# Kernel optimization log

Hardware: AMD Instinct MI355X
Metric: run time of the kernel (lower is better)

## Reference

```python
import jax, jax.numpy as jnp
import numpy as np

N_USER = 50000
N_ITEM = 50000
N = N_USER + N_ITEM
EMB = 64
FEAT = 64
LAYERS = [128, 128]   # input_dim = EMB + FEAT = 128
NNZ = 3_200_000
BATCH = 4096
NEG_SLOPE = 0.2
EPS = 1e-12


def setup_inputs() -> dict:
    key = jax.random.key(0)
    ks = jax.random.split(key, 16)
    inp = {}
    # forward index args
    inp["users"] = jax.random.randint(ks[0], (BATCH,), 0, N_USER)
    inp["pos_items"] = jax.random.randint(ks[1], (BATCH,), 0, N_ITEM)
    inp["neg_items"] = jax.random.randint(ks[2], (BATCH,), 0, N_ITEM)
    # learned embeddings (xavier-ish scale)
    inp["user_emb"] = jax.random.normal(ks[3], (N_USER, EMB), jnp.float32) * 0.1
    inp["item_emb1"] = jax.random.normal(ks[4], (N_ITEM, EMB), jnp.float32) * 0.1
    inp["item_emb2"] = jax.random.normal(ks[5], (N_ITEM, FEAT), jnp.float32) * 0.1
    # fixed user feature matrix (densified sparse feature, non-trainable)
    inp["feature"] = jax.random.normal(ks[6], (N_USER, FEAT), jnp.float32) * 0.1
    # hop-mixing scalar weights w1,w2,w3 (softmax(alpha) at init, then free params)
    alpha = jax.random.normal(ks[7], (3,), jnp.float32)
    inp["w"] = jax.nn.softmax(alpha)
    # per-layer GC / BI weights (all 128x128 here, so stack)
    din = EMB + FEAT
    sc = 1.0 / np.sqrt(din)
    K = len(LAYERS)
    inp["W_gc"] = jax.random.uniform(ks[8], (K, din, LAYERS[0]), jnp.float32, -sc, sc)
    inp["b_gc"] = jax.random.uniform(ks[9], (K, 1, LAYERS[0]), jnp.float32, -sc, sc)
    inp["W_bi"] = jax.random.uniform(ks[10], (K, din, LAYERS[0]), jnp.float32, -sc, sc)
    inp["b_bi"] = jax.random.uniform(ks[11], (K, 1, LAYERS[0]), jnp.float32, -sc, sc)
    # normalized adjacency in COO form (same sparsity pattern for all hops)
    inp["adj_rows"] = jax.random.randint(ks[12], (NNZ,), 0, N)
    inp["adj_cols"] = jax.random.randint(ks[13], (NNZ,), 0, N)
    inp["adj_vals"] = jax.random.uniform(ks[14], (NNZ,), jnp.float32, 0.0, 0.06)
    return inp


def _spmm(vals, rows, cols, X):
    # sparse (N,N) @ dense (N,D) via gather + segment-sum
    return jax.ops.segment_sum(vals[:, None] * X[cols], rows, num_segments=N)


def _forward(users, pos_items, neg_items, user_emb, item_emb1, item_emb2,
             feature, w, W_gc, b_gc, W_bi, b_bi, adj_rows, adj_cols, adj_vals):
    temp = jnp.concatenate([feature, item_emb2], axis=0)            # (N, FEAT)
    ego = jnp.concatenate([user_emb, item_emb1], axis=0)            # (N, EMB)
    ego = jnp.concatenate([ego, temp], axis=1)                      # (N, 128)
    all_emb = [ego]
    # torch `A ** i` cumulative -> elementwise value powers v, v^2, v^6
    v = adj_vals
    comb = w[0] * v + w[1] * (v ** 2) + w[2] * (v ** 6)
    for k in range(len(LAYERS)):
        side = _spmm(comb, adj_rows, adj_cols, ego)                 # (N, 128)
        sum_e = side @ W_gc[k] + b_gc[k]
        bi_e = (ego * side) @ W_bi[k] + b_bi[k]
        ego = jax.nn.leaky_relu(sum_e + bi_e, negative_slope=NEG_SLOPE)
        nrm = jnp.linalg.norm(ego, axis=1, keepdims=True)
        all_emb.append(ego / jnp.maximum(nrm, EPS))                 # F.normalize
    all_e = jnp.concatenate(all_emb, axis=1)                        # (N, 384)
    u_g = all_e[:N_USER][users]
    pos_g = all_e[N_USER:][pos_items]
    neg_g = all_e[N_USER:][neg_items]
    return u_g, pos_g, neg_g


def reference(users, pos_items, neg_items, user_emb, item_emb1, item_emb2,
              feature, w, W_gc, b_gc, W_bi, b_bi, adj_rows, adj_cols, adj_vals):
    return _forward(users, pos_items, neg_items, user_emb, item_emb1, item_emb2,
                    feature, w, W_gc, b_gc, W_bi, b_bi, adj_rows, adj_cols, adj_vals)
```

## Files before the change

### kernel.cpp

```cpp
#include <hip/hip_runtime.h>
#include <math.h>

#define N_USER 50000
#define N_ITEM 50000
#define NTOT   100000
#define D      128
#define BATCH_ 4096
#define NEG_SLOPE 0.2f
#define EPS_ 1e-12f
#define SCAN_CHUNK 1024
#define NBUK 782
#define NCHK 256
#define NSCAN (NBUK * NCHK)
#define BUKCAP 12288

typedef __attribute__((ext_vector_type(8))) short bfrag;
typedef __attribute__((ext_vector_type(4))) float f32x4;

static __device__ __forceinline__ float bf2f(unsigned short h) {
    return __uint_as_float(((unsigned)h) << 16);
}
static __device__ __forceinline__ unsigned short f2bf(float f) {
    unsigned u = __float_as_uint(f);
    u += 0x7fffu + ((u >> 16) & 1u);
    return (unsigned short)(u >> 16);
}

__global__ void assemble_and_pack(const float* __restrict__ user_emb,
                                  const float* __restrict__ item_emb1,
                                  const float* __restrict__ item_emb2,
                                  const float* __restrict__ feature,
                                  const float* __restrict__ W_gc,
                                  const float* __restrict__ W_bi,
                                  unsigned short* __restrict__ ego0h,
                                  unsigned short* __restrict__ Wp) {
    if (blockIdx.x < 32) {
        int t = blockIdx.x * 256 + threadIdx.x;
        int lane  = t & 63;
        int nt    = (t >> 6) & 7;
        int kt    = (t >> 9) & 3;
        int mat   = (t >> 11) & 1;
        int layer = (t >> 12) & 1;
        const float* W = (mat ? W_bi : W_gc) + (size_t)layer * D * D;
        int n = nt * 16 + (lane & 15);
        int kbase = kt * 32 + (lane >> 4) * 8;
        unsigned short o8[8];
        #pragma unroll
        for (int e = 0; e < 8; ++e) o8[e] = f2bf(W[(size_t)(kbase + e) * D + n]);
        *(int4*)(Wp + (size_t)t * 8) = *(int4*)o8;
        return;
    }
    int t = (blockIdx.x - 32) * 256 + threadIdx.x;
    const int total = NTOT * (D / 4);
    if (t >= total) return;
    int row = t >> 5;
    int q   = t & 31;
    int d0  = q * 4;
    const float* src;
    if (d0 < 64) {
        src = (row < N_USER) ? user_emb  + (size_t)row * 64 + d0
                             : item_emb1 + (size_t)(row - N_USER) * 64 + d0;
    } else {
        src = (row < N_USER) ? feature   + (size_t)row * 64 + (d0 - 64)
                             : item_emb2 + (size_t)(row - N_USER) * 64 + (d0 - 64);
    }
    float4 v = *(const float4*)src;
    ushort4 h;
    h.x = f2bf(v.x); h.y = f2bf(v.y); h.z = f2bf(v.z); h.w = f2bf(v.w);
    *(ushort4*)(ego0h + (size_t)row * D + d0) = h;
}

__global__ __launch_bounds__(1024) void hist_buckets(const int* __restrict__ rows,
                                                     int* __restrict__ cnt2,
                                                     int nnz, int chunk_sz) {
    __shared__ int h[NBUK];
    for (int i = threadIdx.x; i < NBUK; i += 1024) h[i] = 0;
    __syncthreads();
    int c = blockIdx.x;
    int base = c * chunk_sz, end = min(base + chunk_sz, nnz);
    for (int e = base + threadIdx.x; e < end; e += 1024)
        atomicAdd(&h[rows[e] >> 7], 1);
    __syncthreads();
    for (int b = threadIdx.x; b < NBUK; b += 1024)
        cnt2[b * NCHK + c] = h[b];
}

__global__ __launch_bounds__(1024) void scan_block_sums(const int* __restrict__ cnt,
                                                        int* __restrict__ bsum, int n) {
    __shared__ int ws[16];
    int i = blockIdx.x * SCAN_CHUNK + threadIdx.x;
    int x = (i < n) ? cnt[i] : 0;
    #pragma unroll
    for (int d = 32; d >= 1; d >>= 1) x += __shfl_xor(x, d);
    int wid = threadIdx.x >> 6, lane = threadIdx.x & 63;
    if (lane == 0) ws[wid] = x;
    __syncthreads();
    if (threadIdx.x == 0) {
        int s = 0;
        #pragma unroll
        for (int k = 0; k < 16; ++k) s += ws[k];
        bsum[blockIdx.x] = s;
    }
}

__global__ void scan_small(const int* __restrict__ bsum, int* __restrict__ boff, int nb) {
    if (threadIdx.x == 0 && blockIdx.x == 0) {
        int acc = 0;
        for (int i = 0; i < nb; ++i) { boff[i] = acc; acc += bsum[i]; }
    }
}

__global__ __launch_bounds__(1024) void scan_chunks(const int* __restrict__ cnt,
                                                    const int* __restrict__ boff,
                                                    int* __restrict__ off, int n) {
    __shared__ int ws[16];
    int tid = threadIdx.x;
    int i = blockIdx.x * SCAN_CHUNK + tid;
    int x = (i < n) ? cnt[i] : 0;
    int v = x;
    #pragma unroll
    for (int d = 1; d < 64; d <<= 1) { int u = __shfl_up(v, d); if ((tid & 63) >= d) v += u; }
    int wid = tid >> 6, lane = tid & 63;
    if (lane == 63) ws[wid] = v;
    __syncthreads();
    if (wid == 0) {
        int s = (lane < 16) ? ws[lane] : 0;
        #pragma unroll
        for (int d = 1; d < 16; d <<= 1) { int u = __shfl_up(s, d); if (lane >= d) s += u; }
        if (lane < 16) ws[lane] = s;
    }
    __syncthreads();
    int woff = (wid == 0) ? 0 : ws[wid - 1];
    if (i < n) off[i] = boff[blockIdx.x] + woff + v - x;
}

__global__ __launch_bounds__(1024) void partition_edges(
        const int* __restrict__ rows, const int* __restrict__ cols,
        const float* __restrict__ vals, const float* __restrict__ w3,
        const int* __restrict__ scanout, int2* __restrict__ tmp8,
        int nnz, int chunk_sz) {
    __shared__ int cur[NBUK];
    int c = blockIdx.x;
    for (int b = threadIdx.x; b < NBUK; b += 1024) cur[b] = scanout[b * NCHK + c];
    __syncthreads();
    const float w0 = w3[0], w1 = w3[1], w2 = w3[2];
    int base = c * chunk_sz, end = min(base + chunk_sz, nnz);
    for (int e = base + threadIdx.x; e < end; e += 1024) {
        int r = rows[e];
        float v = vals[e];
        float v2 = v * v;
        float comb = w0 * v + w1 * v2 + w2 * v2 * v2 * v2;
        int pos = atomicAdd(&cur[r >> 7], 1);
        tmp8[pos] = make_int2(((r & 127) << 17) | cols[e], __float_as_int(comb));
    }
}

__global__ __launch_bounds__(256) void bucket_sort(
        const int2* __restrict__ tmp8, const int* __restrict__ scanout,
        unsigned* __restrict__ edges4, int* __restrict__ row_off, int nnz) {
    __shared__ int hist[128], exc[129], cur[128];
    __shared__ unsigned st[BUKCAP];
    int b = blockIdx.x;
    int lo = scanout[b * NCHK];
    int hi = (b + 1 < NBUK) ? scanout[(b + 1) * NCHK] : nnz;
    int cnt = hi - lo;
    if (threadIdx.x < 128) hist[threadIdx.x] = 0;
    __syncthreads();
    for (int i = lo + threadIdx.x; i < hi; i += 256)
        atomicAdd(&hist[tmp8[i].x >> 17], 1);
    __syncthreads();
    if (threadIdx.x == 0) {
        int a = 0;
        for (int r = 0; r < 128; ++r) { exc[r] = a; a += hist[r]; }
        exc[128] = a;
    }
    __syncthreads();
    if (threadIdx.x < 128) {
        cur[threadIdx.x] = exc[threadIdx.x];
        int grow = b * 128 + threadIdx.x;
        if (grow <= NTOT) row_off[grow] = lo + exc[threadIdx.x];
    }
    __syncthreads();
    if (cnt <= BUKCAP) {
        for (int i = lo + threadIdx.x; i < hi; i += 256) {
            int2 t = tmp8[i];
            int rl = t.x >> 17;
            int p = atomicAdd(&cur[rl], 1);
            unsigned cb = (unsigned)f2bf(__int_as_float(t.y)) & 0x7FFFu;
            st[p] = (cb << 17) | ((unsigned)t.x & 0x1FFFFu);
        }
        __syncthreads();
        for (int i = threadIdx.x; i < cnt; i += 256)
            edges4[lo + i] = st[i];
    } else {
        for (int i = lo + threadIdx.x; i < hi; i += 256) {
            int2 t = tmp8[i];
            int rl = t.x >> 17;
            int p = atomicAdd(&cur[rl], 1);
            unsigned cb = (unsigned)f2bf(__int_as_float(t.y)) & 0x7FFFu;
            edges4[lo + p] = (cb << 17) | ((unsigned)t.x & 0x1FFFFu);
        }
    }
}

__global__ __launch_bounds__(256) void spmm_csr_h(const int* __restrict__ row_off,
                                                  const unsigned* __restrict__ edges4,
                                                  const unsigned short* __restrict__ Xh,
                                                  unsigned short* __restrict__ side_h) {
    int row = (blockIdx.x * blockDim.x + threadIdx.x) >> 6;
    if (row >= NTOT) return;
    int lane = threadIdx.x & 63;
    int g = lane >> 4;
    int q = lane & 15;
    int s = row_off[row], e = row_off[row + 1];

    float a[8];
    #pragma unroll
    for (int j = 0; j < 8; ++j) a[j] = 0.f;

    for (int i = s; i < e; i += 16) {
        int i0 = i + g, i1 = i + 4 + g, i2 = i + 8 + g, i3 = i + 12 + g;
        unsigned e0 = (i0 < e) ? edges4[i0] : 0u;
        unsigned e1 = (i1 < e) ? edges4[i1] : 0u;
        unsigned e2 = (i2 < e) ? edges4[i2] : 0u;
        unsigned e3 = (i3 < e) ? edges4[i3] : 0u;
        float v0 = bf2f((unsigned short)(e0 >> 17));
        float v1 = bf2f((unsigned short)(e1 >> 17));
        float v2 = bf2f((unsigned short)(e2 >> 17));
        float v3 = bf2f((unsigned short)(e3 >> 17));
        int4 x0 = *(const int4*)(Xh + (size_t)(e0 & 0x1FFFFu) * D + q * 8);
        int4 x1 = *(const int4*)(Xh + (size_t)(e1 & 0x1FFFFu) * D + q * 8);
        int4 x2 = *(const int4*)(Xh + (size_t)(e2 & 0x1FFFFu) * D + q * 8);
        int4 x3 = *(const int4*)(Xh + (size_t)(e3 & 0x1FFFFu) * D + q * 8);
        const unsigned short* p0 = (const unsigned short*)&x0;
        const unsigned short* p1 = (const unsigned short*)&x1;
        const unsigned short* p2 = (const unsigned short*)&x2;
        const unsigned short* p3 = (const unsigned short*)&x3;
        #pragma unroll
        for (int j = 0; j < 8; ++j)
            a[j] += v0 * bf2f(p0[j]) + v1 * bf2f(p1[j])
                  + v2 * bf2f(p2[j]) + v3 * bf2f(p3[j]);
    }
    #pragma unroll
    for (int j = 0; j < 8; ++j) {
        a[j] += __shfl_xor(a[j], 16);
        a[j] += __shfl_xor(a[j], 32);
    }
    if (g == 0) {
        unsigned short o[8];
        #pragma unroll
        for (int j = 0; j < 8; ++j) o[j] = f2bf(a[j]);
        *(int4*)(side_h + (size_t)row * D + q * 8) = *(int4*)o;
    }
}

__global__ __launch_bounds__(256) void layer_gemm_mfma(
        const unsigned short* __restrict__ side_h,
        const unsigned short* __restrict__ ego_h,
        const unsigned short* __restrict__ Wp, int layer,
        const float* __restrict__ bgc, const float* __restrict__ bbi,
        unsigned short* __restrict__ ego_out_h, float* __restrict__ norms) {
    __shared__ unsigned short Sl[64 * D];
    __shared__ unsigned short Pl[64 * D];
    __shared__ float sqp[4][64];

    const int r0  = blockIdx.x * 64;
    const int tid = threadIdx.x;
    const int lane = tid & 63;
    const int wv   = tid >> 6;

    #pragma unroll
    for (int it = 0; it < 4; ++it) {
        int c = tid + it * 256;
        int r = c >> 4;
        int q = c & 15;
        int row = r0 + r;
        int4 sv = make_int4(0, 0, 0, 0), ev = make_int4(0, 0, 0, 0);
        if (row < NTOT) {
            sv = *(const int4*)(side_h + (size_t)row * D + q * 8);
            ev = *(const int4*)(ego_h  + (size_t)row * D + q * 8);
        }
        int dst = (r * 256 + q * 16) ^ ((r & 7) << 4);
        *(int4*)((char*)Sl + dst) = sv;
        const unsigned short* sp = (const unsigned short*)&sv;
        const unsigned short* ep = (const unsigned short*)&ev;
        unsigned short pv[8];
        #pragma unroll
        for (int j = 0; j < 8; ++j) pv[j] = f2bf(bf2f(sp[j]) * bf2f(ep[j]));
        *(int4*)((char*)Pl + dst) = *(int4*)pv;
    }

    bfrag wg[4][2], wb[4][2];
    #pragma unroll
    for (int kt = 0; kt < 4; ++kt)
        #pragma unroll
        for (int n2 = 0; n2 < 2; ++n2) {
            int nt = wv * 2 + n2;
            size_t og = ((((size_t)(layer * 2 + 0) * 4 + kt) * 8 + nt) * 64 + lane) * 8;
            size_t ob = ((((size_t)(layer * 2 + 1) * 4 + kt) * 8 + nt) * 64 + lane) * 8;
            wg[kt][n2] = *(const bfrag*)(Wp + og);
            wb[kt][n2] = *(const bfrag*)(Wp + ob);
        }

    __syncthreads();

    f32x4 acc[4][2];
    #pragma unroll
    for (int m = 0; m < 4; ++m)
        #pragma unroll
        for (int n = 0; n < 2; ++n) acc[m][n] = (f32x4){0.f, 0.f, 0.f, 0.f};

    #pragma unroll
    for (int kt = 0; kt < 4; ++kt) {
        bfrag sf[4], pf[4];
        #pragma unroll
        for (int m = 0; m < 4; ++m) {
            int rowl = m * 16 + (lane & 15);
            int byte = (rowl * 256 + kt * 64 + (lane >> 4) * 16) ^ ((rowl & 7) << 4);
            sf[m] = *(const bfrag*)((const char*)Sl + byte);
            pf[m] = *(const bfrag*)((const char*)Pl + byte);
        }
        #pragma unroll
        for (int m = 0; m < 4; ++m)
            #pragma unroll
            for (int n = 0; n < 2; ++n) {
                acc[m][n] = __builtin_amdgcn_mfma_f32_16x16x32_bf16(sf[m], wg[kt][n], acc[m][n], 0, 0, 0);
                acc[m][n] = __builtin_amdgcn_mfma_f32_16x16x32_bf16(pf[m], wb[kt][n], acc[m][n], 0, 0, 0);
            }
    }

    float bsum[2];
    #pragma unroll
    for (int n = 0; n < 2; ++n) {
        int col = wv * 32 + n * 16 + (lane & 15);
        bsum[n] = bgc[col] + bbi[col];
    }

    float sq[4][4];
    #pragma unroll
    for (int m = 0; m < 4; ++m)
        #pragma unroll
        for (int r = 0; r < 4; ++r) sq[m][r] = 0.f;

    #pragma unroll
    for (int m = 0; m < 4; ++m) {
        int rowl = m * 16 + (lane >> 4) * 4;
        #pragma unroll
        for (int n = 0; n < 2; ++n) {
            int col = wv * 32 + n * 16 + (lane & 15);
            #pragma unroll
            for (int r = 0; r < 4; ++r) {
                float o = acc[m][n][r] + bsum[n];
                o = (o > 0.f) ? o : NEG_SLOPE * o;
                sq[m][r] += o * o;
                int row = r0 + rowl + r;
                if (row < NTOT)
                    ego_out_h[(size_t)row * D + col] = f2bf(o);
            }
        }
    }

    #pragma unroll
    for (int m = 0; m < 4; ++m)
        #pragma unroll
        for (int r = 0; r < 4; ++r) {
            float v = sq[m][r];
            #pragma unroll
            for (int off = 8; off >= 1; off >>= 1) v += __shfl_xor(v, off);
            if ((lane & 15) == 0) sqp[wv][m * 16 + (lane >> 4) * 4 + r] = v;
        }
    __syncthreads();
    if (tid < 64) {
        int row = r0 + tid;
        if (row < NTOT) {
            float s = sqp[0][tid] + sqp[1][tid] + sqp[2][tid] + sqp[3][tid];
            norms[row] = fmaxf(sqrtf(s), EPS_);
        }
    }
}

__global__ void gather_out(const int* __restrict__ users,
                           const int* __restrict__ pos,
                           const int* __restrict__ neg,
                           const float* __restrict__ user_emb,
                           const float* __restrict__ item_emb1,
                           const float* __restrict__ item_emb2,
                           const float* __restrict__ feature,
                           const unsigned short* __restrict__ ego1h,
                           const unsigned short* __restrict__ ego2h,
                           const float* __restrict__ n1,
                           const float* __restrict__ n2,
                           float* __restrict__ out) {
    int t = blockIdx.x * blockDim.x + threadIdx.x;
    const int total = 3 * BATCH_ * 384;
    if (t >= total) return;
    int c = t % 384;
    int i = (t / 384) % BATCH_;
    int s = t / (384 * BATCH_);
    int idx  = (s == 0) ? users[i] : (s == 1 ? pos[i] : neg[i]);
    int node = (s == 0) ? idx : idx + N_USER;
    float val;
    if (c < 128) {
        if (s == 0)
            val = (c < 64) ? user_emb[(size_t)idx * 64 + c]
                           : feature[(size_t)idx * 64 + (c - 64)];
        else
            val = (c < 64) ? item_emb1[(size_t)idx * 64 + c]
                           : item_emb2[(size_t)idx * 64 + (c - 64)];
    } else if (c < 256) {
        val = bf2f(ego1h[(size_t)node * D + (c - 128)]) / n1[node];
    } else {
        val = bf2f(ego2h[(size_t)node * D + (c - 256)]) / n2[node];
    }
    out[t] = val;
}

extern "C" void kernel_launch(void* const* d_in, const int* in_sizes, int n_in,
                              void* d_out, int out_size, void* d_ws, size_t ws_size,
                              hipStream_t stream) {
    const int*   users     = (const int*)d_in[0];
    const int*   pos_items = (const int*)d_in[1];
    const int*   neg_items = (const int*)d_in[2];
    const float* user_emb  = (const float*)d_in[3];
    const float* item_emb1 = (const float*)d_in[4];
    const float* item_emb2 = (const float*)d_in[5];
    const float* feature   = (const float*)d_in[6];
    const float* w3        = (const float*)d_in[7];
    const float* W_gc      = (const float*)d_in[8];
    const float* b_gc      = (const float*)d_in[9];
    const float* W_bi      = (const float*)d_in[10];
    const float* b_bi      = (const float*)d_in[11];
    const int*   adj_rows  = (const int*)d_in[12];
    const int*   adj_cols  = (const int*)d_in[13];
    const float* adj_vals  = (const float*)d_in[14];
    const int nnz = in_sizes[14];

    const size_t nd = (size_t)NTOT * D;
    const int NB2 = (NSCAN + SCAN_CHUNK - 1) / SCAN_CHUNK;

    char* p = (char*)d_ws;
    float* n1    = (float*)p;                 p += NTOT * 4;
    float* n2    = (float*)p;                 p += NTOT * 4;
    unsigned short* ego0h  = (unsigned short*)p; p += nd * 2;
    unsigned short* ego1h  = (unsigned short*)p; p += nd * 2;
    unsigned short* ego2h  = (unsigned short*)p; p += nd * 2;
    unsigned short* side_h = (unsigned short*)p; p += nd * 2;
    unsigned short* Wp     = (unsigned short*)p; p += 8192 * 8 * 2;
    int*  row_off = (int*)p;                  p += (NTOT + 128) * 4;
    int*  cnt2    = (int*)p;                  p += (size_t)NSCAN * 4;
    int*  scanout = (int*)p;                  p += (size_t)NSCAN * 4;
    int*  bsum    = (int*)p;                  p += 256 * 4;
    int*  boff    = (int*)p;                  p += 256 * 4;
    int2* tmp8    = (int2*)p;                 p += (size_t)nnz * 8;
    unsigned* edges4 = (unsigned*)p;          p += (size_t)nnz * 4;

    float* out = (float*)d_out;

    {
        int ablocks = (NTOT * (D / 4) + 255) / 256;
        assemble_and_pack<<<32 + ablocks, 256, 0, stream>>>(
            user_emb, item_emb1, item_emb2, feature, W_gc, W_bi, ego0h, Wp);
    }

    int chunk_sz = (nnz + NCHK - 1) / NCHK;
    hist_buckets<<<NCHK, 1024, 0, stream>>>(adj_rows, cnt2, nnz, chunk_sz);
    scan_block_sums<<<NB2, SCAN_CHUNK, 0, stream>>>(cnt2, bsum, NSCAN);
    scan_small<<<1, 64, 0, stream>>>(bsum, boff, NB2);
    scan_chunks<<<NB2, SCAN_CHUNK, 0, stream>>>(cnt2, boff, scanout, NSCAN);
    partition_edges<<<NCHK, 1024, 0, stream>>>(adj_rows, adj_cols, adj_vals, w3,
                                               scanout, tmp8, nnz, chunk_sz);
    bucket_sort<<<NBUK, 256, 0, stream>>>(tmp8, scanout, edges4, row_off, nnz);

    for (int k = 0; k < 2; ++k) {
        const unsigned short* Xh = (k == 0) ? ego0h : ego1h;
        unsigned short* egoNh    = (k == 0) ? ego1h : ego2h;
        float* nrm               = (k == 0) ? n1 : n2;

        spmm_csr_h<<<(NTOT + 3) / 4, 256, 0, stream>>>(row_off, edges4, Xh, side_h);
        layer_gemm_mfma<<<(NTOT + 63) / 64, 256, 0, stream>>>(
            side_h, Xh, Wp, k,
            b_gc + (size_t)k * D, b_bi + (size_t)k * D,
            egoNh, nrm);
    }

    {
        int total = 3 * BATCH_ * 384;
        gather_out<<<(total + 255) / 256, 256, 0, stream>>>(
            users, pos_items, neg_items,
            user_emb, item_emb1, item_emb2, feature,
            ego1h, ego2h, n1, n2, out);
    }
}
```

Baseline: 376.2 us.

## Pad CSR rows to multiples of eight and drop bounds checks in SpMM

The bucket sort now rounds each row's edge count up to a multiple of eight and zero-fills the padding, placing each bucket at a padded global offset. This lets the SpMM inner loop process eight edges per iteration without per-edge bounds checks. The loop also decodes bf16 values with shifts and masks and computes gather addresses with a shift-or. The tradeoffs are extra padded edges to gather (zero weight reads row 0), a larger edges buffer, and a smaller shared staging capacity, so more buckets may take the global-memory fallback.

```diff
diff --git a/kernel.cpp b/kernel.cpp
--- a/kernel.cpp
+++ b/kernel.cpp
@@ -12,7 +12,8 @@
 #define NBUK 782
 #define NCHK 256
 #define NSCAN (NBUK * NCHK)
-#define BUKCAP 12288
+#define PADS 904
+#define BUKCAP 5632
 
 typedef __attribute__((ext_vector_type(8))) short bfrag;
 typedef __attribute__((ext_vector_type(4))) float f32x4;
@@ -24,6 +25,10 @@
     unsigned u = __float_as_uint(f);
     u += 0x7fffu + ((u >> 16) & 1u);
     return (unsigned short)(u >> 16);
+}
+static __device__ __forceinline__ int lpad(const int* scanout, int b, int nnz) {
+    int base = (b < NBUK) ? scanout[b * NCHK] : nnz;
+    return (base + b * PADS + 7) & ~7;
 }
 
 __global__ void assemble_and_pack(const float* __restrict__ user_emb,
@@ -158,47 +163,59 @@
 __global__ __launch_bounds__(256) void bucket_sort(
         const int2* __restrict__ tmp8, const int* __restrict__ scanout,
         unsigned* __restrict__ edges4, int* __restrict__ row_off, int nnz) {
-    __shared__ int hist[128], exc[129], cur[128];
+    __shared__ int hist[128];
+    __shared__ int excp[129];
+    __shared__ int curp[128];
     __shared__ unsigned st[BUKCAP];
+    const int tid = threadIdx.x;
     int b = blockIdx.x;
     int lo = scanout[b * NCHK];
     int hi = (b + 1 < NBUK) ? scanout[(b + 1) * NCHK] : nnz;
-    int cnt = hi - lo;
-    if (threadIdx.x < 128) hist[threadIdx.x] = 0;
-    __syncthreads();
-    for (int i = lo + threadIdx.x; i < hi; i += 256)
+    int lpb  = lpad(scanout, b, nnz);
+    int lpb1 = lpad(scanout, b + 1, nnz);
+    int space = lpb1 - lpb;
+
+    if (tid < 128) hist[tid] = 0;
+    __syncthreads();
+    for (int i = lo + tid; i < hi; i += 256)
         atomicAdd(&hist[tmp8[i].x >> 17], 1);
     __syncthreads();
-    if (threadIdx.x == 0) {
+    if (tid == 0) {
         int a = 0;
-        for (int r = 0; r < 128; ++r) { exc[r] = a; a += hist[r]; }
-        exc[128] = a;
-    }
-    __syncthreads();
-    if (threadIdx.x < 128) {
-        cur[threadIdx.x] = exc[threadIdx.x];
-        int grow = b * 128 + threadIdx.x;
-        if (grow <= NTOT) row_off[grow] = lo + exc[threadIdx.x];
-    }
-    __syncthreads();
-    if (cnt <= BUKCAP) {
-        for (int i = lo + threadIdx.x; i < hi; i += 256) {
+        #pragma unroll
+        for (int r = 0; r < 128; ++r) { excp[r] = a; a += (hist[r] + 7) & ~7; }
+        excp[128] = a;
+    }
+    __syncthreads();
+    if (tid < 128) {
+        curp[tid] = excp[tid];
+        int grow = b * 128 + tid;
+        if (grow <= NTOT) row_off[grow] = lpb + excp[tid];
+    }
+    __syncthreads();
+
+    if (space <= BUKCAP) {
+        for (int i = tid; i < space; i += 256) st[i] = 0u;
+        __syncthreads();
+        for (int i = lo + tid; i < hi; i += 256) {
             int2 t = tmp8[i];
             int rl = t.x >> 17;
-            int p = atomicAdd(&cur[rl], 1);
+            int p = atomicAdd(&curp[rl], 1);
             unsigned cb = (unsigned)f2bf(__int_as_float(t.y)) & 0x7FFFu;
             st[p] = (cb << 17) | ((unsigned)t.x & 0x1FFFFu);
         }
         __syncthreads();
-        for (int i = threadIdx.x; i < cnt; i += 256)
-            edges4[lo + i] = st[i];
+        for (int i = tid; i < space; i += 256)
+            edges4[lpb + i] = st[i];
     } else {
-        for (int i = lo + threadIdx.x; i < hi; i += 256) {
+        for (int i = tid; i < space; i += 256) edges4[lpb + i] = 0u;
+        __syncthreads();
+        for (int i = lo + tid; i < hi; i += 256) {
             int2 t = tmp8[i];
             int rl = t.x >> 17;
-            int p = atomicAdd(&cur[rl], 1);
+            int p = atomicAdd(&curp[rl], 1);
             unsigned cb = (unsigned)f2bf(__int_as_float(t.y)) & 0x7FFFu;
-            edges4[lo + p] = (cb << 17) | ((unsigned)t.x & 0x1FFFFu);
+            edges4[lpb + p] = (cb << 17) | ((unsigned)t.x & 0x1FFFFu);
         }
     }
 }
@@ -213,33 +230,29 @@
     int g = lane >> 4;
     int q = lane & 15;
     int s = row_off[row], e = row_off[row + 1];
+    const unsigned qoff = (unsigned)(q << 4);
+    const char* Xb = (const char*)Xh;
 
     float a[8];
     #pragma unroll
     for (int j = 0; j < 8; ++j) a[j] = 0.f;
 
-    for (int i = s; i < e; i += 16) {
-        int i0 = i + g, i1 = i + 4 + g, i2 = i + 8 + g, i3 = i + 12 + g;
-        unsigned e0 = (i0 < e) ? edges4[i0] : 0u;
-        unsigned e1 = (i1 < e) ? edges4[i1] : 0u;
-        unsigned e2 = (i2 < e) ? edges4[i2] : 0u;
-        unsigned e3 = (i3 < e) ? edges4[i3] : 0u;
-        float v0 = bf2f((unsigned short)(e0 >> 17));
-        float v1 = bf2f((unsigned short)(e1 >> 17));
-        float v2 = bf2f((unsigned short)(e2 >> 17));
-        float v3 = bf2f((unsigned short)(e3 >> 17));
-        int4 x0 = *(const int4*)(Xh + (size_t)(e0 & 0x1FFFFu) * D + q * 8);
-        int4 x1 = *(const int4*)(Xh + (size_t)(e1 & 0x1FFFFu) * D + q * 8);
-        int4 x2 = *(const int4*)(Xh + (size_t)(e2 & 0x1FFFFu) * D + q * 8);
-        int4 x3 = *(const int4*)(Xh + (size_t)(e3 & 0x1FFFFu) * D + q * 8);
-        const unsigned short* p0 = (const unsigned short*)&x0;
-        const unsigned short* p1 = (const unsigned short*)&x1;
-        const unsigned short* p2 = (const unsigned short*)&x2;
-        const unsigned short* p3 = (const unsigned short*)&x3;
-        #pragma unroll
-        for (int j = 0; j < 8; ++j)
-            a[j] += v0 * bf2f(p0[j]) + v1 * bf2f(p1[j])
-                  + v2 * bf2f(p2[j]) + v3 * bf2f(p3[j]);
+    for (int i = s; i < e; i += 8) {
+        unsigned e0 = edges4[i + g];
+        unsigned e1 = edges4[i + 4 + g];
+        float v0 = __uint_as_float((e0 >> 1) & 0x7FFF0000u);
+        float v1 = __uint_as_float((e1 >> 1) & 0x7FFF0000u);
+        int4 x0 = *(const int4*)(Xb + (((e0 & 0x1FFFFu) << 8) | qoff));
+        int4 x1 = *(const int4*)(Xb + (((e1 & 0x1FFFFu) << 8) | qoff));
+        const unsigned* w0 = (const unsigned*)&x0;
+        const unsigned* w1 = (const unsigned*)&x1;
+        #pragma unroll
+        for (int k = 0; k < 4; ++k) {
+            a[2 * k]     += v0 * __uint_as_float(w0[k] << 16)
+                          + v1 * __uint_as_float(w1[k] << 16);
+            a[2 * k + 1] += v0 * __uint_as_float(w0[k] & 0xFFFF0000u)
+                          + v1 * __uint_as_float(w1[k] & 0xFFFF0000u);
+        }
     }
     #pragma unroll
     for (int j = 0; j < 8; ++j) {
@@ -437,6 +450,7 @@
 
     const size_t nd = (size_t)NTOT * D;
     const int NB2 = (NSCAN + SCAN_CHUNK - 1) / SCAN_CHUNK;
+    const size_t edges_cap = (size_t)nnz + (size_t)NBUK * PADS + 64;
 
     char* p = (char*)d_ws;
     float* n1    = (float*)p;                 p += NTOT * 4;
@@ -452,7 +466,7 @@
     int*  bsum    = (int*)p;                  p += 256 * 4;
     int*  boff    = (int*)p;                  p += 256 * 4;
     int2* tmp8    = (int2*)p;                 p += (size_t)nnz * 8;
-    unsigned* edges4 = (unsigned*)p;          p += (size_t)nnz * 4;
+    unsigned* edges4 = (unsigned*)p;          p += edges_cap * 4;
 
     float* out = (float*)d_out;
 
```

Result: slower. 689.9 us (+83.4%).

## Split ego embeddings into column halves and run SpMM per half

Applied to the files above, without the earlier changes.

Stores the bf16 ego embeddings as two planar 64-column halves (each NTOT x 64) instead of interleaved 128-column rows. The SpMM now runs twice per layer, once per half, with 8 edge groups of 8 lanes each, so each pass gathers from a 12.8 MB table. The intent is to make the random gather working set fit in cache. The cost is reading the edge list twice and launching an extra kernel. The GEMM, pack and gather-out kernels are updated to the new addressing.

```diff
diff --git a/kernel.cpp b/kernel.cpp
--- a/kernel.cpp
+++ b/kernel.cpp
@@ -5,6 +5,7 @@
 #define N_ITEM 50000
 #define NTOT   100000
 #define D      128
+#define HD     64
 #define BATCH_ 4096
 #define NEG_SLOPE 0.2f
 #define EPS_ 1e-12f
@@ -13,6 +14,7 @@
 #define NCHK 256
 #define NSCAN (NBUK * NCHK)
 #define BUKCAP 12288
+#define HSZ ((size_t)NTOT * HD)
 
 typedef __attribute__((ext_vector_type(8))) short bfrag;
 typedef __attribute__((ext_vector_type(4))) float f32x4;
@@ -67,7 +69,8 @@
     float4 v = *(const float4*)src;
     ushort4 h;
     h.x = f2bf(v.x); h.y = f2bf(v.y); h.z = f2bf(v.z); h.w = f2bf(v.w);
-    *(ushort4*)(ego0h + (size_t)row * D + d0) = h;
+    int half = d0 >> 6;
+    *(ushort4*)(ego0h + (size_t)half * HSZ + (size_t)row * HD + (d0 & 63)) = h;
 }
 
 __global__ __launch_bounds__(1024) void hist_buckets(const int* __restrict__ rows,
@@ -203,15 +206,16 @@
     }
 }
 
-__global__ __launch_bounds__(256) void spmm_csr_h(const int* __restrict__ row_off,
-                                                  const unsigned* __restrict__ edges4,
-                                                  const unsigned short* __restrict__ Xh,
-                                                  unsigned short* __restrict__ side_h) {
+__global__ __launch_bounds__(256) void spmm_csr_half(const int* __restrict__ row_off,
+                                                     const unsigned* __restrict__ edges4,
+                                                     const unsigned short* __restrict__ Xhalf,
+                                                     unsigned short* __restrict__ side_h,
+                                                     int half) {
     int row = (blockIdx.x * blockDim.x + threadIdx.x) >> 6;
     if (row >= NTOT) return;
     int lane = threadIdx.x & 63;
-    int g = lane >> 4;
-    int q = lane & 15;
+    int g = lane >> 3;
+    int q = lane & 7;
     int s = row_off[row], e = row_off[row + 1];
 
     float a[8];
@@ -219,30 +223,22 @@
     for (int j = 0; j < 8; ++j) a[j] = 0.f;
 
     for (int i = s; i < e; i += 16) {
-        int i0 = i + g, i1 = i + 4 + g, i2 = i + 8 + g, i3 = i + 12 + g;
+        int i0 = i + g, i1 = i + 8 + g;
         unsigned e0 = (i0 < e) ? edges4[i0] : 0u;
         unsigned e1 = (i1 < e) ? edges4[i1] : 0u;
-        unsigned e2 = (i2 < e) ? edges4[i2] : 0u;
-        unsigned e3 = (i3 < e) ? edges4[i3] : 0u;
         float v0 = bf2f((unsigned short)(e0 >> 17));
         float v1 = bf2f((unsigned short)(e1 >> 17));
-        float v2 = bf2f((unsigned short)(e2 >> 17));
-        float v3 = bf2f((unsigned short)(e3 >> 17));
-        int4 x0 = *(const int4*)(Xh + (size_t)(e0 & 0x1FFFFu) * D + q * 8);
-        int4 x1 = *(const int4*)(Xh + (size_t)(e1 & 0x1FFFFu) * D + q * 8);
-        int4 x2 = *(const int4*)(Xh + (size_t)(e2 & 0x1FFFFu) * D + q * 8);
-        int4 x3 = *(const int4*)(Xh + (size_t)(e3 & 0x1FFFFu) * D + q * 8);
+        int4 x0 = *(const int4*)(Xhalf + (size_t)(e0 & 0x1FFFFu) * HD + q * 8);
+        int4 x1 = *(const int4*)(Xhalf + (size_t)(e1 & 0x1FFFFu) * HD + q * 8);
         const unsigned short* p0 = (const unsigned short*)&x0;
         const unsigned short* p1 = (const unsigned short*)&x1;
-        const unsigned short* p2 = (const unsigned short*)&x2;
-        const unsigned short* p3 = (const unsigned short*)&x3;
         #pragma unroll
         for (int j = 0; j < 8; ++j)
-            a[j] += v0 * bf2f(p0[j]) + v1 * bf2f(p1[j])
-                  + v2 * bf2f(p2[j]) + v3 * bf2f(p3[j]);
+            a[j] += v0 * bf2f(p0[j]) + v1 * bf2f(p1[j]);
     }
     #pragma unroll
     for (int j = 0; j < 8; ++j) {
+        a[j] += __shfl_xor(a[j], 8);
         a[j] += __shfl_xor(a[j], 16);
         a[j] += __shfl_xor(a[j], 32);
     }
@@ -250,7 +246,7 @@
         unsigned short o[8];
         #pragma unroll
         for (int j = 0; j < 8; ++j) o[j] = f2bf(a[j]);
-        *(int4*)(side_h + (size_t)row * D + q * 8) = *(int4*)o;
+        *(int4*)(side_h + (size_t)row * D + half * HD + q * 8) = *(int4*)o;
     }
 }
 
@@ -278,7 +274,7 @@
         int4 sv = make_int4(0, 0, 0, 0), ev = make_int4(0, 0, 0, 0);
         if (row < NTOT) {
             sv = *(const int4*)(side_h + (size_t)row * D + q * 8);
-            ev = *(const int4*)(ego_h  + (size_t)row * D + q * 8);
+            ev = *(const int4*)(ego_h + (size_t)(q >> 3) * HSZ + (size_t)row * HD + (q & 7) * 8);
         }
         int dst = (r * 256 + q * 16) ^ ((r & 7) << 4);
         *(int4*)((char*)Sl + dst) = sv;
@@ -348,6 +344,7 @@
         #pragma unroll
         for (int n = 0; n < 2; ++n) {
             int col = wv * 32 + n * 16 + (lane & 15);
+            size_t cbase = (size_t)(col >> 6) * HSZ + (col & 63);
             #pragma unroll
             for (int r = 0; r < 4; ++r) {
                 float o = acc[m][n][r] + bsum[n];
@@ -355,7 +352,7 @@
                 sq[m][r] += o * o;
                 int row = r0 + rowl + r;
                 if (row < NTOT)
-                    ego_out_h[(size_t)row * D + col] = f2bf(o);
+                    ego_out_h[cbase + (size_t)row * HD] = f2bf(o);
             }
         }
     }
@@ -408,9 +405,11 @@
             val = (c < 64) ? item_emb1[(size_t)idx * 64 + c]
                            : item_emb2[(size_t)idx * 64 + (c - 64)];
     } else if (c < 256) {
-        val = bf2f(ego1h[(size_t)node * D + (c - 128)]) / n1[node];
+        int cc = c - 128;
+        val = bf2f(ego1h[(size_t)(cc >> 6) * HSZ + (size_t)node * HD + (cc & 63)]) / n1[node];
     } else {
-        val = bf2f(ego2h[(size_t)node * D + (c - 256)]) / n2[node];
+        int cc = c - 256;
+        val = bf2f(ego2h[(size_t)(cc >> 6) * HSZ + (size_t)node * HD + (cc & 63)]) / n2[node];
     }
     out[t] = val;
 }
@@ -476,7 +475,10 @@
         unsigned short* egoNh    = (k == 0) ? ego1h : ego2h;
         float* nrm               = (k == 0) ? n1 : n2;
 
-        spmm_csr_h<<<(NTOT + 3) / 4, 256, 0, stream>>>(row_off, edges4, Xh, side_h);
+        spmm_csr_half<<<(NTOT + 3) / 4, 256, 0, stream>>>(
+            row_off, edges4, Xh, side_h, 0);
+        spmm_csr_half<<<(NTOT + 3) / 4, 256, 0, stream>>>(
+            row_off, edges4, Xh + HSZ, side_h, 1);
         layer_gemm_mfma<<<(NTOT + 63) / 64, 256, 0, stream>>>(
             side_h, Xh, Wp, k,
             b_gc + (size_t)k * D, b_bi + (size_t)k * D,
```

Result: slower. 390.7 us (+3.8%).
